# Optimization experiments

Hardware: AMD Instinct MI355X
Metric: run time of the kernel (lower is better)

## Reference

```python
import jax, jax.numpy as jnp
import numpy as np

N, F, H, R, T, E, C = 50000, 128, 64, 3, 2, 500000, 2


def _seg_sum(v, idx, n):
    return jax.ops.segment_sum(v, idx, num_segments=n)


def _sage(x, src, dst, Wl, Wr, b, n):
    # PyG SAGEConv(mean): lin_l(mean_{j->i} x_j) + lin_r(x_i); lin_l carries bias.
    s = _seg_sum(x[src], dst, n)
    cnt = _seg_sum(jnp.ones((src.shape[0],), x.dtype), dst, n)
    agg = s / jnp.maximum(cnt, 1.0)[:, None]
    return agg @ Wl + x @ Wr + b


def _gcn(x, src, dst, w, W, b, n):
    # PyG GCNConv with edge_weight: self-loops (weight 1) + symmetric norm.
    deg = _seg_sum(w, dst, n) + 1.0
    dinv = deg ** -0.5
    norm = dinv[src] * w * dinv[dst]
    xW = x @ W
    return _seg_sum(norm[:, None] * xW[src], dst, n) + xW / deg[:, None] + b


def setup_inputs() -> dict:
    key = jax.random.key(0)
    ks = jax.random.split(key, 32)
    rn = lambda k, shp, s=0.1: jax.random.normal(k, shp, dtype=jnp.float32) * s
    return {
        "x": rn(ks[0], (N, F), 1.0),
        "edge_main": jax.random.randint(ks[1], (R, 2, E), 0, N, dtype=jnp.int32),
        "edge_tree": jax.random.randint(ks[2], (R, T, 2, E), 0, N, dtype=jnp.int32),
        "sage_Wl0": rn(ks[3], (R, F, H)), "sage_Wr0": rn(ks[4], (R, F, H)), "sage_b0": rn(ks[5], (R, H)),
        "sage_Wl1": rn(ks[6], (R, H, H)), "sage_Wr1": rn(ks[7], (R, H, H)), "sage_b1": rn(ks[8], (R, H)),
        "tree_Wl": rn(ks[9], (R, T, F, H)), "tree_Wr": rn(ks[10], (R, T, F, H)), "tree_b": rn(ks[11], (R, T, H)),
        "gate_W": rn(ks[12], (R, T, H)), "gate_b": rn(ks[13], (R, T)),
        "node_emb": rn(ks[14], (R, H), 1.0), "edge_emb": rn(ks[15], (R, H), 1.0),
        "fm_W": rn(ks[16], (R, 2 * H + F, F)), "fm_b": rn(ks[17], (R, F)),
        "ea_W1": rn(ks[18], (3 * H, F)), "ea_b1": rn(ks[19], (F,)),
        "ea_W2": rn(ks[20], (F, 1)), "ea_b2": rn(ks[21], (1,)),
        "gcn_W0": rn(ks[22], (R, F, H)), "gcn_b0": rn(ks[23], (R, H)),
        "gcn_W1": rn(ks[24], (R, H, H)), "gcn_b1": rn(ks[25], (R, H)),
        "lin_W": rn(ks[26], (R * H, C)), "lin_b": rn(ks[27], (C,)),
    }


def reference(x, edge_main, edge_tree, sage_Wl0, sage_Wr0, sage_b0, sage_Wl1, sage_Wr1, sage_b1,
              tree_Wl, tree_Wr, tree_b, gate_W, gate_b, node_emb, edge_emb, fm_W, fm_b,
              ea_W1, ea_b1, ea_W2, ea_b2, gcn_W0, gcn_b0, gcn_W1, gcn_b1, lin_W, lin_b):
    outs = []
    for r in range(R):
        src, dst = edge_main[r, 0], edge_main[r, 1]
        # Layer_AGG main SAGE stack (2 layers, relu between; dropout = eval no-op)
        y = jax.nn.relu(_sage(x, src, dst, sage_Wl0[r], sage_Wr0[r], sage_b0[r], N))
        y = _sage(y, src, dst, sage_Wl1[r], sage_Wr1[r], sage_b1[r], N)
        # tree branches + softmax gating
        trees = []
        for t in range(T):
            ts, td = edge_tree[r, t, 0], edge_tree[r, t, 1]
            trees.append(jax.nn.relu(_sage(x, ts, td, tree_Wl[r, t], tree_Wr[r, t], tree_b[r, t], N)))
        gates = jnp.stack([trees[t] @ gate_W[r, t] + gate_b[r, t] for t in range(T)], axis=-1)  # [N,T]
        alpha = jax.nn.softmax(gates, axis=-1)
        x_tree = sum(trees[t] * alpha[:, t:t + 1] for t in range(T))
        lo = y + 1.0 * x_tree  # self.weight = 1
        # edge mask via edge_attr_mlp on [lo[src], lo[dst], edge_type_emb]
        ef = jnp.concatenate([lo[src], lo[dst], jnp.broadcast_to(edge_emb[r], (E, H))], axis=-1)
        em = jax.nn.relu(ef @ ea_W1 + ea_b1) @ ea_W2 + ea_b2  # [E,1]
        # feature mask via feat_mask_r on [lo, x, node_type_emb]
        hetro = jnp.concatenate([lo, x, jnp.broadcast_to(node_emb[r], (N, H))], axis=-1)
        fm = hetro @ fm_W[r] + fm_b[r]
        mx = x * fm
        w = ((em - em.min()) / (em.max() - em.min()))[:, 0]  # min-max norm -> [E]
        # hetero GCN stack with edge weights
        z = jax.nn.relu(_gcn(mx, src, dst, w, gcn_W0[r], gcn_b0[r], N))
        z = _gcn(z, src, dst, w, gcn_W1[r], gcn_b1[r], N)
        outs.append(z)
    x_temp = jnp.concatenate(outs, axis=1)  # [N, R*H]
    logits = jnp.clip(x_temp @ lin_W + lin_b, -1e10, 1e10)
    return jax.nn.log_softmax(logits, axis=1), x_temp
```

## Files before the change

### kernel.cpp

```cpp
#include <hip/hip_runtime.h>
#include <cstdint>

#define N_NODES 50000
#define FEAT    128
#define HID     64
#define NREL    3
#define NTREE   2
#define NEDGE   500000
#define NCLS    2

#define BKT   391
#define CAP   1600
#define CHUNK 4096

typedef __attribute__((ext_vector_type(8))) short bfrag;
typedef __attribute__((ext_vector_type(4))) float ffrag;

__device__ __forceinline__ float wave_red(float v){
  #pragma unroll
  for(int off = 32; off > 0; off >>= 1) v += __shfl_xor(v, off, 64);
  return v;
}

__device__ __forceinline__ unsigned short f2b(float f){
  unsigned int u = __float_as_uint(f);
  unsigned int r = (u + 0x7FFFu + ((u >> 16) & 1u)) >> 16;
  return (unsigned short)r;
}
__device__ __forceinline__ float b2f_lo(unsigned int u){ return __uint_as_float(u << 16); }
__device__ __forceinline__ float b2f_hi(unsigned int u){ return __uint_as_float(u & 0xFFFF0000u); }
__device__ __forceinline__ float b2f(unsigned short s){ return __uint_as_float(((unsigned int)s) << 16); }
__device__ __forceinline__ unsigned int pk2(float lo, float hi){
  return ((unsigned int)f2b(hi) << 16) | f2b(lo);
}

struct EdgePtrs { const int* s[9]; const int* d[9]; };

__global__ __launch_bounds__(256)
void k_passA(EdgePtrs ep, int* __restrict__ cursor, int* __restrict__ bucketed){
  int set = blockIdx.y;
  const int* src = ep.s[set];
  const int* dst = ep.d[set];
  __shared__ int stage[CHUNK];
  __shared__ int hist[BKT], gbase[BKT], lbase[BKT], cur[BKT];
  int tid = threadIdx.x;
  for(int b = tid; b < BKT; b += 256) hist[b] = 0;
  __syncthreads();
  int e0 = blockIdx.x * CHUNK;
  int nE = NEDGE - e0; if(nE > CHUNK) nE = CHUNK;
  for(int i = tid; i < nE; i += 256) atomicAdd(&hist[dst[e0 + i] >> 7], 1);
  __syncthreads();
  for(int b = tid; b < BKT; b += 256){
    int c = hist[b];
    gbase[b] = c ? atomicAdd(&cursor[set * BKT + b], c) : 0;
  }
  if(tid < 64){
    int running = 0;
    for(int base = 0; base < BKT; base += 64){
      int idx = base + tid;
      int v = (idx < BKT) ? hist[idx] : 0;
      int orig = v;
      #pragma unroll
      for(int off = 1; off < 64; off <<= 1){
        int t = __shfl_up(v, off, 64);
        if(tid >= off) v += t;
      }
      if(idx < BKT){ lbase[idx] = running + v - orig; cur[idx] = running + v - orig; }
      running += __shfl(v, 63, 64);
    }
  }
  __syncthreads();
  for(int i = tid; i < nE; i += 256){
    int e = e0 + i;
    int d = dst[e];
    int r = atomicAdd(&cur[d >> 7], 1);
    stage[r] = (d << 16) | src[e];
  }
  __syncthreads();
  int* bk = bucketed + (size_t)set * BKT * CAP;
  for(int i = tid; i < nE; i += 256){
    int p = stage[i];
    int b = ((unsigned int)p) >> 23;
    int pos = gbase[b] + (i - lbase[b]);
    if(pos < CAP) bk[b * CAP + pos] = p;
  }
}

__global__ void k_scanB(const int* __restrict__ cursor, int* __restrict__ bktbase,
                        int* __restrict__ indptr9){
  int set = blockIdx.x;
  __shared__ int sm[512];
  int tid = threadIdx.x;
  int v = (tid < BKT) ? cursor[set * BKT + tid] : 0;
  sm[tid] = v; __syncthreads();
  for(int off = 1; off < 512; off <<= 1){
    int t = (tid >= off) ? sm[tid - off] : 0;
    __syncthreads();
    sm[tid] += t;
    __syncthreads();
  }
  if(tid < BKT) bktbase[set * BKT + tid] = sm[tid] - v;
  if(tid == 0) indptr9[(size_t)set * (N_NODES + 1) + N_NODES] = NEDGE;
}

__global__ __launch_bounds__(256)
void k_passB(const int* __restrict__ bucketed, const int* __restrict__ cursor,
             const int* __restrict__ bktbase, int* __restrict__ indptr9,
             int* __restrict__ csr9){
  int set = blockIdx.y, b = blockIdx.x;
  int cnt = cursor[set * BKT + b]; if(cnt > CAP) cnt = CAP;
  int ebase = bktbase[set * BKT + b];
  const int* bk = bucketed + (size_t)set * BKT * CAP + b * CAP;
  __shared__ int pk[CAP];
  __shared__ int stage[CAP];
  __shared__ int h[128], sc[128], cur[128];
  int tid = threadIdx.x;
  for(int i = tid; i < cnt; i += 256) pk[i] = bk[i];
  if(tid < 128) h[tid] = 0;
  __syncthreads();
  for(int i = tid; i < cnt; i += 256) atomicAdd(&h[(pk[i] >> 16) & 127], 1);
  __syncthreads();
  if(tid < 128) sc[tid] = h[tid];
  __syncthreads();
  for(int off = 1; off < 128; off <<= 1){
    int t = 0;
    if(tid < 128 && tid >= off) t = sc[tid - off];
    __syncthreads();
    if(tid < 128) sc[tid] += t;
    __syncthreads();
  }
  if(tid < 128){
    int excl = sc[tid] - h[tid];
    cur[tid] = excl;
    int node = b * 128 + tid;
    if(node < N_NODES) indptr9[(size_t)set * (N_NODES + 1) + node] = ebase + excl;
  }
  __syncthreads();
  for(int i = tid; i < cnt; i += 256){
    int p = pk[i];
    int r = atomicAdd(&cur[(p >> 16) & 127], 1);
    stage[r] = p & 0xFFFF;
  }
  __syncthreads();
  int* out = csr9 + (size_t)set * NEDGE + ebase;
  for(int i = tid; i < cnt; i += 256) out[i] = stage[i];
}

__global__ void k_tobf16(const float* __restrict__ in, unsigned short* __restrict__ o, int n4){
  int i = blockIdx.x * 256 + threadIdx.x;
  if(i < n4){
    float4 v = ((const float4*)in)[i];
    ushort4 u; u.x = f2b(v.x); u.y = f2b(v.y); u.z = f2b(v.z); u.w = f2b(v.w);
    ((ushort4*)o)[i] = u;
  }
}

struct PackJobs { const float* src[20]; int wst[20]; int K[20]; int dst[20]; int n; };

__global__ void k_wpack(PackJobs J, unsigned short* __restrict__ out){
  int j = blockIdx.x;
  if(j >= J.n) return;
  const float* s = J.src[j];
  int wst = J.wst[j], K = J.K[j];
  unsigned short* o = out + J.dst[j];
  for(int i = threadIdx.x; i < K * 64; i += 256){
    int k = i >> 6, c = i & 63;
    o[((((k >> 3) * 64) + c) << 3) + (k & 7)] = f2b(s[(size_t)k * wst + c]);
  }
}

struct MG {
  const unsigned short* Wt[4];
  const float* bias[4];
  const void* add[4];
  const float* mul[4];
  void* out[4];
  int ast, mst, ost;
};

template<int K1, int NGRP, int OUT_BF16>
__global__ __launch_bounds__(256)
void k_mgemm(const unsigned short* __restrict__ X1, int xs1, MG P){
  constexpr int KS = K1 / 32;
  int tid = threadIdx.x;
  int lane = tid & 63;
  int w = tid >> 6;
  int row0 = blockIdx.x * 64 + w * 16;
  int l15 = lane & 15, kg = lane >> 4;
  int arow = row0 + l15; if(arow > N_NODES - 1) arow = N_NODES - 1;
  bfrag a[KS];
  #pragma unroll
  for(int ks = 0; ks < KS; ks++)
    a[ks] = *(const bfrag*)(X1 + (size_t)arow * xs1 + ks * 32 + kg * 8);
  int orow0 = row0 + kg * 4;
  #pragma unroll
  for(int g = 0; g < NGRP; g++){
    const unsigned short* Wg = P.Wt[g];
    #pragma unroll
    for(int ct = 0; ct < 4; ct++){
      int col = ct * 16 + l15;
      ffrag acc = {0.f, 0.f, 0.f, 0.f};
      #pragma unroll
      for(int ks = 0; ks < KS; ks++){
        bfrag bf = *(const bfrag*)(Wg + (((size_t)(ks * 4 + kg) * 64 + col) << 3));
        acc = __builtin_amdgcn_mfma_f32_16x16x32_bf16(a[ks], bf, acc, 0, 0, 0);
      }
      #pragma unroll
      for(int i = 0; i < 4; i++){
        int r = orow0 + i;
        if(r >= N_NODES) break;
        float v = acc[i];
        if(OUT_BF16) ((unsigned short*)P.out[g])[(size_t)r * P.ost + col] = f2b(v);
        else         ((float*)P.out[g])[(size_t)r * P.ost + col] = v;
      }
    }
  }
}

struct S23 {
  const unsigned short* Wr[3];
  const float* bias[3];
  const unsigned short* ag3;
  const unsigned short* Wl1;
  unsigned short *y0, *t0, *t1, *tbs;
};

__global__ __launch_bounds__(256)
void k_s23(const unsigned short* __restrict__ xb, S23 P){
  __shared__ unsigned short ytile[64][72];
  int tid = threadIdx.x, lane = tid & 63, w = tid >> 6;
  int row0 = blockIdx.x * 64 + w * 16;
  int l15 = lane & 15, kg = lane >> 4;
  int arow = row0 + l15; if(arow > N_NODES - 1) arow = N_NODES - 1;
  bfrag a[4];
  #pragma unroll
  for(int ks = 0; ks < 4; ks++)
    a[ks] = *(const bfrag*)(xb + (size_t)arow * 128 + ks * 32 + kg * 8);
  int orow0 = row0 + kg * 4;
  #pragma unroll
  for(int g = 0; g < 3; g++){
    const unsigned short* Wg = P.Wr[g];
    unsigned short* og = (g == 0) ? P.y0 : (g == 1) ? P.t0 : P.t1;
    #pragma unroll
    for(int ct = 0; ct < 4; ct++){
      int col = ct * 16 + l15;
      ffrag acc = {0.f, 0.f, 0.f, 0.f};
      #pragma unroll
      for(int ks = 0; ks < 4; ks++){
        bfrag bf = *(const bfrag*)(Wg + (((size_t)(ks * 4 + kg) * 64 + col) << 3));
        acc = __builtin_amdgcn_mfma_f32_16x16x32_bf16(a[ks], bf, acc, 0, 0, 0);
      }
      float bv = P.bias[g][col];
      #pragma unroll
      for(int i = 0; i < 4; i++){
        int r = orow0 + i;
        int rr = (r < N_NODES) ? r : N_NODES - 1;
        float v = acc[i] + bv + b2f(P.ag3[(size_t)g * N_NODES * 64 + (size_t)rr * 64 + col]);
        v = fmaxf(v, 0.f);
        unsigned short hh = f2b(v);
        if(g == 0) ytile[w * 16 + kg * 4 + i][col] = hh;
        if(r < N_NODES) og[(size_t)r * 64 + col] = hh;
      }
    }
  }
  __syncthreads();
  bfrag a2[2];
  a2[0] = *(const bfrag*)&ytile[w * 16 + l15][kg * 8];
  a2[1] = *(const bfrag*)&ytile[w * 16 + l15][32 + kg * 8];
  #pragma unroll
  for(int ct = 0; ct < 4; ct++){
    int col = ct * 16 + l15;
    ffrag acc = {0.f, 0.f, 0.f, 0.f};
    bfrag b0 = *(const bfrag*)(P.Wl1 + (((size_t)(0 * 4 + kg) * 64 + col) << 3));
    bfrag b1 = *(const bfrag*)(P.Wl1 + (((size_t)(1 * 4 + kg) * 64 + col) << 3));
    acc = __builtin_amdgcn_mfma_f32_16x16x32_bf16(a2[0], b0, acc, 0, 0, 0);
    acc = __builtin_amdgcn_mfma_f32_16x16x32_bf16(a2[1], b1, acc, 0, 0, 0);
    #pragma unroll
    for(int i = 0; i < 4; i++){
      int r = orow0 + i;
      if(r >= N_NODES) break;
      P.tbs[(size_t)r * 64 + col] = f2b(acc[i]);
    }
  }
}

struct YG {
  const unsigned short* Wr1;
  const float* b1;
  const float* AG;
  const unsigned short *t0b, *t1b;
  const float *gate_W, *gate_b;
  unsigned short* lo;
  const float *ee, *ne, *eaW1, *eab1, *fmW, *fmb;
  float *cE, *cF;
  int ggm;
};

__global__ __launch_bounds__(256)
void k_ygates(const unsigned short* __restrict__ y0b, YG P){
  if(blockIdx.x >= P.ggm){
    int which = blockIdx.x - P.ggm;
    int j = threadIdx.x;
    if(j < 128){
      if(which == 0){
        float s = P.eab1[j];
        for(int k = 0; k < 64; k++) s += P.ee[k] * P.eaW1[(128 + k) * 128 + j];
        P.cE[j] = s;
      } else {
        float s = P.fmb[j];
        for(int k = 0; k < 64; k++) s += P.ne[k] * P.fmW[(192 + k) * 128 + j];
        P.cF[j] = s;
      }
    }
    return;
  }
  int tid = threadIdx.x, lane = tid & 63, w = tid >> 6;
  int row0 = blockIdx.x * 64 + w * 16;
  int l15 = lane & 15, kg = lane >> 4;
  int arow = row0 + l15; if(arow > N_NODES - 1) arow = N_NODES - 1;
  bfrag a0f = *(const bfrag*)(y0b + (size_t)arow * 64 + kg * 8);
  bfrag a1f = *(const bfrag*)(y0b + (size_t)arow * 64 + 32 + kg * 8);
  int orow0 = row0 + kg * 4;
  float vv[4][4], t0v[4][4], t1v[4][4];
  float gw0[4], gw1[4];
  #pragma unroll
  for(int ct = 0; ct < 4; ct++){
    int col = ct * 16 + l15;
    gw0[ct] = P.gate_W[col];
    gw1[ct] = P.gate_W[64 + col];
  }
  #pragma unroll
  for(int ct = 0; ct < 4; ct++){
    int col = ct * 16 + l15;
    ffrag acc = {0.f, 0.f, 0.f, 0.f};
    bfrag b0 = *(const bfrag*)(P.Wr1 + (((size_t)(0 * 4 + kg) * 64 + col) << 3));
    bfrag b1 = *(const bfrag*)(P.Wr1 + (((size_t)(1 * 4 + kg) * 64 + col) << 3));
    acc = __builtin_amdgcn_mfma_f32_16x16x32_bf16(a0f, b0, acc, 0, 0, 0);
    acc = __builtin_amdgcn_mfma_f32_16x16x32_bf16(a1f, b1, acc, 0, 0, 0);
    float bv = P.b1[col];
    #pragma unroll
    for(int i = 0; i < 4; i++){
      int r = orow0 + i;
      int rr = (r < N_NODES) ? r : N_NODES - 1;
      vv[i][ct] = acc[i] + bv + P.AG[(size_t)rr * 64 + col];
      t0v[i][ct] = b2f(P.t0b[(size_t)rr * 64 + col]);
      t1v[i][ct] = b2f(P.t1b[(size_t)rr * 64 + col]);
    }
  }
  float pg0[4] = {0.f, 0.f, 0.f, 0.f}, pg1[4] = {0.f, 0.f, 0.f, 0.f};
  #pragma unroll
  for(int i = 0; i < 4; i++)
    #pragma unroll
    for(int ct = 0; ct < 4; ct++){
      pg0[i] += t0v[i][ct] * gw0[ct];
      pg1[i] += t1v[i][ct] * gw1[ct];
    }
  #pragma unroll
  for(int off = 1; off < 16; off <<= 1){
    #pragma unroll
    for(int i = 0; i < 4; i++){
      pg0[i] += __shfl_xor(pg0[i], off, 64);
      pg1[i] += __shfl_xor(pg1[i], off, 64);
    }
  }
  float gb0 = P.gate_b[0], gb1 = P.gate_b[1];
  #pragma unroll
  for(int i = 0; i < 4; i++){
    int r = orow0 + i;
    if(r >= N_NODES) break;
    float g0 = pg0[i] + gb0, g1 = pg1[i] + gb1;
    float m = fmaxf(g0, g1);
    float e0 = expf(g0 - m), e1 = expf(g1 - m);
    float av = e0 / (e0 + e1);
    #pragma unroll
    for(int ct = 0; ct < 4; ct++){
      int col = ct * 16 + l15;
      P.lo[(size_t)r * 64 + col] = f2b(vv[i][ct] + av * t0v[i][ct] + (1.f - av) * t1v[i][ct]);
    }
  }
}

struct ABMX2 {
  const unsigned short* Wea[4];
  const unsigned short* Wfm[2];
  const unsigned short* G0;
  const float* cF;
  const float* xf32;
  unsigned short* ab;
  unsigned short* xw0;
};

__global__ __launch_bounds__(256)
void k_abmx2(const unsigned short* __restrict__ LOb, const unsigned short* __restrict__ xb, ABMX2 P){
  __shared__ unsigned short mxtile[64][136];
  int tid = threadIdx.x, lane = tid & 63, w = tid >> 6;
  int row0 = blockIdx.x * 64 + w * 16;
  int l15 = lane & 15, kg = lane >> 4;
  int arow = row0 + l15; if(arow > N_NODES - 1) arow = N_NODES - 1;
  bfrag a[6];
  a[0] = *(const bfrag*)(LOb + (size_t)arow * 64 + kg * 8);
  a[1] = *(const bfrag*)(LOb + (size_t)arow * 64 + 32 + kg * 8);
  #pragma unroll
  for(int ks = 0; ks < 4; ks++)
    a[2 + ks] = *(const bfrag*)(xb + (size_t)arow * 128 + ks * 32 + kg * 8);
  int orow0 = row0 + kg * 4;
  #pragma unroll
  for(int g = 0; g < 4; g++){
    const unsigned short* Wg = P.Wea[g];
    #pragma unroll
    for(int ct = 0; ct < 4; ct++){
      int col = ct * 16 + l15;
      ffrag acc = {0.f, 0.f, 0.f, 0.f};
      bfrag b0 = *(const bfrag*)(Wg + (((size_t)(0 * 4 + kg) * 64 + col) << 3));
      bfrag b1 = *(const bfrag*)(Wg + (((size_t)(1 * 4 + kg) * 64 + col) << 3));
      acc = __builtin_amdgcn_mfma_f32_16x16x32_bf16(a[0], b0, acc, 0, 0, 0);
      acc = __builtin_amdgcn_mfma_f32_16x16x32_bf16(a[1], b1, acc, 0, 0, 0);
      #pragma unroll
      for(int i = 0; i < 4; i++){
        int r = orow0 + i;
        if(r >= N_NODES) break;
        P.ab[(size_t)r * 256 + g * 64 + col] = f2b(acc[i]);
      }
    }
  }
  #pragma unroll
  for(int g = 0; g < 2; g++){
    const unsigned short* Wg = P.Wfm[g];
    #pragma unroll
    for(int ct = 0; ct < 4; ct++){
      int col = ct * 16 + l15;
      ffrag acc = {0.f, 0.f, 0.f, 0.f};
      #pragma unroll
      for(int ks = 0; ks < 6; ks++){
        bfrag bf = *(const bfrag*)(Wg + (((size_t)(ks * 4 + kg) * 64 + col) << 3));
        acc = __builtin_amdgcn_mfma_f32_16x16x32_bf16(a[ks], bf, acc, 0, 0, 0);
      }
      float bv = P.cF[g * 64 + col];
      #pragma unroll
      for(int i = 0; i < 4; i++){
        int r = orow0 + i;
        int rr = (r < N_NODES) ? r : N_NODES - 1;
        float v = (acc[i] + bv) * P.xf32[(size_t)rr * 128 + g * 64 + col];
        mxtile[w * 16 + kg * 4 + i][g * 64 + col] = f2b(v);
      }
    }
  }
  __syncthreads();
  bfrag a3[4];
  #pragma unroll
  for(int ks = 0; ks < 4; ks++)
    a3[ks] = *(const bfrag*)&mxtile[w * 16 + l15][ks * 32 + kg * 8];
  #pragma unroll
  for(int ct = 0; ct < 4; ct++){
    int col = ct * 16 + l15;
    ffrag acc = {0.f, 0.f, 0.f, 0.f};
    #pragma unroll
    for(int ks = 0; ks < 4; ks++){
      bfrag bf = *(const bfrag*)(P.G0 + (((size_t)(ks * 4 + kg) * 64 + col) << 3));
      acc = __builtin_amdgcn_mfma_f32_16x16x32_bf16(a3[ks], bf, acc, 0, 0, 0);
    }
    #pragma unroll
    for(int i = 0; i < 4; i++){
      int r = orow0 + i;
      if(r >= N_NODES) break;
      P.xw0[(size_t)r * 64 + col] = f2b(acc[i]);
    }
  }
}

template<int OUTB>
__global__ void k_aggq(const unsigned short* __restrict__ TB, int tst,
                       const int* __restrict__ indptr, const int* __restrict__ csr,
                       void* __restrict__ out){
  int br = blockIdx.y;
  const unsigned short* T = TB + (size_t)br * tst;
  const int* ip = indptr + (size_t)br * (N_NODES + 1);
  const int* cs = csr + (size_t)br * NEDGE;
  int lane = threadIdx.x & 63, wid = threadIdx.x >> 6;
  int node = blockIdx.x * 4 + wid;
  if(node >= N_NODES) return;
  int q = lane >> 4, c = lane & 15;
  int beg = ip[node], end = ip[node + 1];
  int cnt = end - beg;
  float sc = 1.0f / (float)(cnt >= 1 ? cnt : 1);
  float a0 = 0.f, a1 = 0.f, a2 = 0.f, a3 = 0.f;
  int j = beg + q;
  for(; j + 4 < end; j += 8){
    int s0 = cs[j], s1 = cs[j + 4];
    uint2 u0 = *(const uint2*)(T + (size_t)s0 * 64 + c * 4);
    uint2 u1 = *(const uint2*)(T + (size_t)s1 * 64 + c * 4);
    a0 += b2f_lo(u0.x) + b2f_lo(u1.x); a1 += b2f_hi(u0.x) + b2f_hi(u1.x);
    a2 += b2f_lo(u0.y) + b2f_lo(u1.y); a3 += b2f_hi(u0.y) + b2f_hi(u1.y);
  }
  if(j < end){
    int s = cs[j];
    uint2 u = *(const uint2*)(T + (size_t)s * 64 + c * 4);
    a0 += b2f_lo(u.x); a1 += b2f_hi(u.x);
    a2 += b2f_lo(u.y); a3 += b2f_hi(u.y);
  }
  a0 += __shfl_xor(a0, 16, 64); a1 += __shfl_xor(a1, 16, 64);
  a2 += __shfl_xor(a2, 16, 64); a3 += __shfl_xor(a3, 16, 64);
  a0 += __shfl_xor(a0, 32, 64); a1 += __shfl_xor(a1, 32, 64);
  a2 += __shfl_xor(a2, 32, 64); a3 += __shfl_xor(a3, 32, 64);
  if(q == 0){
    if(OUTB){
      ushort4 o; o.x = f2b(a0 * sc); o.y = f2b(a1 * sc); o.z = f2b(a2 * sc); o.w = f2b(a3 * sc);
      *(ushort4*)((unsigned short*)out + (size_t)br * tst + (size_t)node * 64 + c * 4) = o;
    } else {
      *(float4*)((float*)out + (size_t)node * 64 + c * 4) = float4{a0 * sc, a1 * sc, a2 * sc, a3 * sc};
    }
  }
}

__global__ void k_em2(const unsigned short* __restrict__ AB,
                      const int* __restrict__ indptr, const int* __restrict__ csr_src,
                      const float* __restrict__ cvec, const float* __restrict__ W2,
                      const float* __restrict__ b2, float* __restrict__ em,
                      float* __restrict__ sumem, float* __restrict__ pmn, float* __restrict__ pmx){
  int lane = threadIdx.x & 63, wid = threadIdx.x >> 6;
  int node = blockIdx.x * 4 + wid;
  float mn = 3.4e38f, mx = -3.4e38f;
  if(node < N_NODES){
    int q = lane >> 4, c = lane & 15;
    uint4 bu = *(const uint4*)(AB + (size_t)node * 256 + 128 + c * 8);
    float4 cva = *(const float4*)&cvec[c * 8];
    float4 cvb = *(const float4*)&cvec[c * 8 + 4];
    float4 wva = *(const float4*)&W2[c * 8];
    float4 wvb = *(const float4*)&W2[c * 8 + 4];
    float cc0 = b2f_lo(bu.x) + cva.x, cc1 = b2f_hi(bu.x) + cva.y;
    float cc2 = b2f_lo(bu.y) + cva.z, cc3 = b2f_hi(bu.y) + cva.w;
    float cc4 = b2f_lo(bu.z) + cvb.x, cc5 = b2f_hi(bu.z) + cvb.y;
    float cc6 = b2f_lo(bu.w) + cvb.z, cc7 = b2f_hi(bu.w) + cvb.w;
    float b2v = b2[0];
    int beg = indptr[node], end = indptr[node + 1];
    float ssum = 0.f;
    int j = beg + q;
    for(; j + 4 < end; j += 8){
      int s0 = csr_src[j], s1 = csr_src[j + 4];
      uint4 u0 = *(const uint4*)(AB + (size_t)s0 * 256 + c * 8);
      uint4 u1 = *(const uint4*)(AB + (size_t)s1 * 256 + c * 8);
      float v0 = fmaxf(b2f_lo(u0.x) + cc0, 0.f) * wva.x + fmaxf(b2f_hi(u0.x) + cc1, 0.f) * wva.y
               + fmaxf(b2f_lo(u0.y) + cc2, 0.f) * wva.z + fmaxf(b2f_hi(u0.y) + cc3, 0.f) * wva.w
               + fmaxf(b2f_lo(u0.z) + cc4, 0.f) * wvb.x + fmaxf(b2f_hi(u0.z) + cc5, 0.f) * wvb.y
               + fmaxf(b2f_lo(u0.w) + cc6, 0.f) * wvb.z + fmaxf(b2f_hi(u0.w) + cc7, 0.f) * wvb.w;
      float v1 = fmaxf(b2f_lo(u1.x) + cc0, 0.f) * wva.x + fmaxf(b2f_hi(u1.x) + cc1, 0.f) * wva.y
               + fmaxf(b2f_lo(u1.y) + cc2, 0.f) * wva.z + fmaxf(b2f_hi(u1.y) + cc3, 0.f) * wva.w
               + fmaxf(b2f_lo(u1.z) + cc4, 0.f) * wvb.x + fmaxf(b2f_hi(u1.z) + cc5, 0.f) * wvb.y
               + fmaxf(b2f_lo(u1.w) + cc6, 0.f) * wvb.z + fmaxf(b2f_hi(u1.w) + cc7, 0.f) * wvb.w;
      #pragma unroll
      for(int off = 1; off < 16; off <<= 1){
        v0 += __shfl_xor(v0, off, 64);
        v1 += __shfl_xor(v1, off, 64);
      }
      float r0 = v0 + b2v, r1 = v1 + b2v;
      if(c == 0){ em[j] = r0; em[j + 4] = r1; }
      ssum += r0 + r1;
      mn = fminf(mn, fminf(r0, r1)); mx = fmaxf(mx, fmaxf(r0, r1));
    }
    if(j < end){
      int s = csr_src[j];
      uint4 u = *(const uint4*)(AB + (size_t)s * 256 + c * 8);
      float v = fmaxf(b2f_lo(u.x) + cc0, 0.f) * wva.x + fmaxf(b2f_hi(u.x) + cc1, 0.f) * wva.y
              + fmaxf(b2f_lo(u.y) + cc2, 0.f) * wva.z + fmaxf(b2f_hi(u.y) + cc3, 0.f) * wva.w
              + fmaxf(b2f_lo(u.z) + cc4, 0.f) * wvb.x + fmaxf(b2f_hi(u.z) + cc5, 0.f) * wvb.y
              + fmaxf(b2f_lo(u.w) + cc6, 0.f) * wvb.z + fmaxf(b2f_hi(u.w) + cc7, 0.f) * wvb.w;
      #pragma unroll
      for(int off = 1; off < 16; off <<= 1) v += __shfl_xor(v, off, 64);
      float r = v + b2v;
      if(c == 0) em[j] = r;
      ssum += r;
      mn = fminf(mn, r); mx = fmaxf(mx, r);
    }
    ssum += __shfl_xor(ssum, 16, 64); ssum += __shfl_xor(ssum, 32, 64);
    mn = fminf(mn, __shfl_xor(mn, 16, 64)); mn = fminf(mn, __shfl_xor(mn, 32, 64));
    mx = fmaxf(mx, __shfl_xor(mx, 16, 64)); mx = fmaxf(mx, __shfl_xor(mx, 32, 64));
    if(lane == 0) sumem[node] = ssum;
  }
  __shared__ float bmn[4], bmx[4];
  if(lane == 0){ bmn[wid] = mn; bmx[wid] = mx; }
  __syncthreads();
  if(threadIdx.x == 0){
    pmn[blockIdx.x] = fminf(fminf(bmn[0], bmn[1]), fminf(bmn[2], bmn[3]));
    pmx[blockIdx.x] = fmaxf(fmaxf(bmx[0], bmx[1]), fmaxf(bmx[2], bmx[3]));
  }
}

__global__ void k_dinv2(const int* __restrict__ indptr, const float* __restrict__ sumem,
                        const float* __restrict__ pmn, const float* __restrict__ pmx, int nb,
                        float* __restrict__ scal, float* __restrict__ dinv){
  __shared__ float smn[256], smx[256];
  int tid = threadIdx.x;
  float mn = 3.4e38f, mx = -3.4e38f;
  for(int i = tid; i < nb; i += 256){
    mn = fminf(mn, pmn[i]); mx = fmaxf(mx, pmx[i]);
  }
  smn[tid] = mn; smx[tid] = mx; __syncthreads();
  for(int s = 128; s > 0; s >>= 1){
    if(tid < s){ smn[tid] = fminf(smn[tid], smn[tid + s]); smx[tid] = fmaxf(smx[tid], smx[tid + s]); }
    __syncthreads();
  }
  float mn0 = smn[0];
  float inv = 1.0f / fmaxf(smx[0] - mn0, 1e-30f);
  if(blockIdx.x == 0 && tid == 0){ scal[0] = mn0; scal[1] = inv; }
  int i = blockIdx.x * 256 + tid;
  if(i >= N_NODES) return;
  float cnt = (float)(indptr[i + 1] - indptr[i]);
  dinv[i] = rsqrtf(1.f + (sumem[i] - cnt * mn0) * inv);
}

template<int RELU, int OUTB>
__global__ void k_gcn(const unsigned short* __restrict__ xW, const int* __restrict__ indptr,
                      const int* __restrict__ csr_src, const float* __restrict__ em,
                      const float* __restrict__ scal, const float* __restrict__ dinv,
                      const float* __restrict__ bias, void* __restrict__ out, int ostride){
  int lane = threadIdx.x & 63, wid = threadIdx.x >> 6;
  int node = blockIdx.x * 4 + wid;
  if(node >= N_NODES) return;
  int q = lane >> 3, c = lane & 7;
  float mn = scal[0], inv = scal[1];
  float di = dinv[node];
  float a0=0.f,a1=0.f,a2=0.f,a3=0.f,a4=0.f,a5=0.f,a6=0.f,a7=0.f;
  int beg = indptr[node], end = indptr[node + 1];
  int j = beg + q;
  for(; j + 8 < end; j += 16){
    int s0 = csr_src[j], s1 = csr_src[j + 8];
    float w0 = (em[j] - mn) * inv * dinv[s0];
    float w1 = (em[j + 8] - mn) * inv * dinv[s1];
    uint4 u0 = *(const uint4*)(xW + (size_t)s0 * 64 + c * 8);
    uint4 u1 = *(const uint4*)(xW + (size_t)s1 * 64 + c * 8);
    a0 += w0 * b2f_lo(u0.x) + w1 * b2f_lo(u1.x); a1 += w0 * b2f_hi(u0.x) + w1 * b2f_hi(u1.x);
    a2 += w0 * b2f_lo(u0.y) + w1 * b2f_lo(u1.y); a3 += w0 * b2f_hi(u0.y) + w1 * b2f_hi(u1.y);
    a4 += w0 * b2f_lo(u0.z) + w1 * b2f_lo(u1.z); a5 += w0 * b2f_hi(u0.z) + w1 * b2f_hi(u1.z);
    a6 += w0 * b2f_lo(u0.w) + w1 * b2f_lo(u1.w); a7 += w0 * b2f_hi(u0.w) + w1 * b2f_hi(u1.w);
  }
  if(j < end){
    int s = csr_src[j];
    float wv = (em[j] - mn) * inv * dinv[s];
    uint4 u = *(const uint4*)(xW + (size_t)s * 64 + c * 8);
    a0 += wv * b2f_lo(u.x); a1 += wv * b2f_hi(u.x);
    a2 += wv * b2f_lo(u.y); a3 += wv * b2f_hi(u.y);
    a4 += wv * b2f_lo(u.z); a5 += wv * b2f_hi(u.z);
    a6 += wv * b2f_lo(u.w); a7 += wv * b2f_hi(u.w);
  }
  #pragma unroll
  for(int off = 8; off < 64; off <<= 1){
    a0 += __shfl_xor(a0, off, 64); a1 += __shfl_xor(a1, off, 64);
    a2 += __shfl_xor(a2, off, 64); a3 += __shfl_xor(a3, off, 64);
    a4 += __shfl_xor(a4, off, 64); a5 += __shfl_xor(a5, off, 64);
    a6 += __shfl_xor(a6, off, 64); a7 += __shfl_xor(a7, off, 64);
  }
  if(q == 0){
    uint4 su = *(const uint4*)(xW + (size_t)node * 64 + c * 8);
    float4 bva = *(const float4*)&bias[c * 8];
    float4 bvb = *(const float4*)&bias[c * 8 + 4];
    float dd = di * di;
    float r0 = a0 * di + b2f_lo(su.x) * dd + bva.x;
    float r1 = a1 * di + b2f_hi(su.x) * dd + bva.y;
    float r2 = a2 * di + b2f_lo(su.y) * dd + bva.z;
    float r3 = a3 * di + b2f_hi(su.y) * dd + bva.w;
    float r4 = a4 * di + b2f_lo(su.z) * dd + bvb.x;
    float r5 = a5 * di + b2f_hi(su.z) * dd + bvb.y;
    float r6 = a6 * di + b2f_lo(su.w) * dd + bvb.z;
    float r7 = a7 * di + b2f_hi(su.w) * dd + bvb.w;
    if(RELU){
      r0 = fmaxf(r0, 0.f); r1 = fmaxf(r1, 0.f); r2 = fmaxf(r2, 0.f); r3 = fmaxf(r3, 0.f);
      r4 = fmaxf(r4, 0.f); r5 = fmaxf(r5, 0.f); r6 = fmaxf(r6, 0.f); r7 = fmaxf(r7, 0.f);
    }
    if(OUTB){
      uint4 o;
      o.x = pk2(r0, r1); o.y = pk2(r2, r3); o.z = pk2(r4, r5); o.w = pk2(r6, r7);
      *(uint4*)((unsigned short*)out + (size_t)node * ostride + c * 8) = o;
    } else {
      float* o = (float*)out + (size_t)node * ostride + c * 8;
      *(float4*)o       = float4{r0, r1, r2, r3};
      *(float4*)(o + 4) = float4{r4, r5, r6, r7};
    }
  }
}

__global__ void k_logits(const float* __restrict__ xt, const float* __restrict__ lin_W,
                         const float* __restrict__ lin_b, float* __restrict__ out){
  int lane = threadIdx.x & 63, wid = threadIdx.x >> 6;
  int node = blockIdx.x * 4 + wid;
  if(node >= N_NODES) return;
  float a0 = 0.f, a1 = 0.f;
  #pragma unroll
  for(int q = 0; q < 3; q++){
    int k = q * 64 + lane;
    float v = xt[(size_t)node * 192 + k];
    a0 += v * lin_W[k * 2 + 0];
    a1 += v * lin_W[k * 2 + 1];
  }
  a0 = wave_red(a0);
  a1 = wave_red(a1);
  if(lane == 0){
    float l0 = fminf(fmaxf(a0 + lin_b[0], -1e10f), 1e10f);
    float l1 = fminf(fmaxf(a1 + lin_b[1], -1e10f), 1e10f);
    float m = fmaxf(l0, l1);
    float d = expf(l0 - m) + expf(l1 - m);
    float ls = m + logf(d);
    out[(size_t)node * 2 + 0] = l0 - ls;
    out[(size_t)node * 2 + 1] = l1 - ls;
  }
}

extern "C" void kernel_launch(void* const* d_in, const int* in_sizes, int n_in,
                              void* d_out, int out_size, void* d_ws, size_t ws_size,
                              hipStream_t stream){
  (void)in_sizes; (void)n_in; (void)out_size;
  const int N = N_NODES, E = NEDGE;

  const float* x        = (const float*)d_in[0];
  const int*  edge_main = (const int*)d_in[1];
  const int*  edge_tree = (const int*)d_in[2];
  const float* sage_Wl0 = (const float*)d_in[3];
  const float* sage_Wr0 = (const float*)d_in[4];
  const float* sage_b0  = (const float*)d_in[5];
  const float* sage_Wl1 = (const float*)d_in[6];
  const float* sage_Wr1 = (const float*)d_in[7];
  const float* sage_b1  = (const float*)d_in[8];
  const float* tree_Wl  = (const float*)d_in[9];
  const float* tree_Wr  = (const float*)d_in[10];
  const float* tree_b   = (const float*)d_in[11];
  const float* gate_W   = (const float*)d_in[12];
  const float* gate_b   = (const float*)d_in[13];
  const float* node_emb = (const float*)d_in[14];
  const float* edge_emb = (const float*)d_in[15];
  const float* fm_W     = (const float*)d_in[16];
  const float* fm_b     = (const float*)d_in[17];
  const float* ea_W1    = (const float*)d_in[18];
  const float* ea_b1    = (const float*)d_in[19];
  const float* ea_W2    = (const float*)d_in[20];
  const float* ea_b2    = (const float*)d_in[21];
  const float* gcn_W0   = (const float*)d_in[22];
  const float* gcn_b0   = (const float*)d_in[23];
  const float* gcn_W1   = (const float*)d_in[24];
  const float* gcn_b1   = (const float*)d_in[25];
  const float* lin_W    = (const float*)d_in[26];
  const float* lin_b    = (const float*)d_in[27];

  float* out_lsm   = (float*)d_out;
  float* out_xtemp = (float*)d_out + (size_t)N * NCLS;

  char* ws = (char*)d_ws;
  unsigned short* TB3  = (unsigned short*)(ws + 0);
  unsigned short* TBs  = (unsigned short*)(ws + 0);
  unsigned short* AB   = (unsigned short*)(ws + 0);
  unsigned short* AG3  = (unsigned short*)(ws + 19200000);
  float*          AG   = (float*)(ws + 19200000);
  unsigned short* LOb  = (unsigned short*)(ws + 32000000);
  unsigned short* y0b  = (unsigned short*)(ws + 38400000);
  unsigned short* xW0b = (unsigned short*)(ws + 38400000);
  unsigned short* T0b  = (unsigned short*)(ws + 44800000);
  unsigned short* z0b  = (unsigned short*)(ws + 44800000);
  unsigned short* T1b  = (unsigned short*)(ws + 51200000);
  unsigned short* xW1b = (unsigned short*)(ws + 51200000);
  unsigned short* xb   = (unsigned short*)(ws + 57600000);
  int*   bucketed = (int*)(ws + 0);
  unsigned short* Wpk = (unsigned short*)(ws + 70400000);
  int*   csr9     = (int*)(ws + 71000064);
  int*   indptr9  = (int*)(ws + 89000064);
  float* em       = (float*)(ws + 90800128);
  float* sumem    = (float*)(ws + 92800128);
  float* dinv     = (float*)(ws + 93000128);
  int*   cursor   = (int*)(ws + 93200128);
  int*   bktbase  = (int*)(ws + 93214208);
  float* cvecE    = (float*)(ws + 93228288);
  float* cvecF    = (float*)(ws + 93228800);
  float* scal     = (float*)(ws + 93229312);
  float* pmn      = (float*)(ws + 93229568);
  float* pmx      = (float*)(ws + 93279568);
  if(ws_size < 93330000) return;

  const int GN4 = (N + 3) / 4;
  const int GN  = (N + 255) / 256;
  const int GGM = (N + 63) / 64;
  const int NCH = (E + CHUNK - 1) / CHUNK;

  PackJobs PJ[2]; PJ[0].n = 0; PJ[1].n = 0;
  int npj = 0, dstElem = 0;
  const unsigned short* WlpA[NREL]; const unsigned short* WlpB[NREL]; const unsigned short* WlpC[NREL];
  const unsigned short* Wr0j[NREL]; const unsigned short* WrT0[NREL]; const unsigned short* WrT1[NREL];
  const unsigned short* Wl1j[NREL]; const unsigned short* Wr1j[NREL];
  const unsigned short* Fm0j[NREL]; const unsigned short* Fm1j[NREL];
  const unsigned short* G0j[NREL];  const unsigned short* G1j[NREL];
  const unsigned short *EaA0, *EaA1, *EaB0, *EaB1;
  auto addjob = [&](const float* src, int wst, int K) -> const unsigned short* {
    int slot = npj < 20 ? 0 : 1;
    int k = npj - slot * 20;
    PJ[slot].src[k] = src; PJ[slot].wst[k] = wst; PJ[slot].K[k] = K; PJ[slot].dst[k] = dstElem;
    PJ[slot].n = k + 1;
    const unsigned short* ret = Wpk + dstElem;
    dstElem += K * 64; npj++;
    return ret;
  };
  for(int r = 0; r < NREL; r++){
    WlpA[r] = addjob(sage_Wl0 + (size_t)r * 8192, 64, 128);
    WlpB[r] = addjob(tree_Wl + (size_t)(r * NTREE + 0) * 8192, 64, 128);
    WlpC[r] = addjob(tree_Wl + (size_t)(r * NTREE + 1) * 8192, 64, 128);
    Wr0j[r] = addjob(sage_Wr0 + (size_t)r * 8192, 64, 128);
    WrT0[r] = addjob(tree_Wr + (size_t)(r * NTREE + 0) * 8192, 64, 128);
    WrT1[r] = addjob(tree_Wr + (size_t)(r * NTREE + 1) * 8192, 64, 128);
    Wl1j[r] = addjob(sage_Wl1 + (size_t)r * 4096, 64, 64);
    Wr1j[r] = addjob(sage_Wr1 + (size_t)r * 4096, 64, 64);
    Fm0j[r] = addjob(fm_W + (size_t)r * 32768, 128, 192);
    Fm1j[r] = addjob(fm_W + (size_t)r * 32768 + 64, 128, 192);
    G0j[r]  = addjob(gcn_W0 + (size_t)r * 8192, 64, 128);
    G1j[r]  = addjob(gcn_W1 + (size_t)r * 4096, 64, 64);
  }
  EaA0 = addjob(ea_W1, 128, 64);
  EaA1 = addjob(ea_W1 + 64, 128, 64);
  EaB0 = addjob(ea_W1 + 64 * 128, 128, 64);
  EaB1 = addjob(ea_W1 + 64 * 128 + 64, 128, 64);

  EdgePtrs ep;
  for(int r = 0; r < NREL; r++){
    ep.s[r * 3 + 0] = edge_main + (size_t)r * 2 * E;
    ep.d[r * 3 + 0] = ep.s[r * 3 + 0] + E;
    for(int t = 0; t < NTREE; t++){
      ep.s[r * 3 + 1 + t] = edge_tree + ((size_t)(r * NTREE + t) * 2) * E;
      ep.d[r * 3 + 1 + t] = ep.s[r * 3 + 1 + t] + E;
    }
  }
  hipMemsetAsync(cursor, 0, 9 * BKT * 4, stream);
  k_passA<<<dim3(NCH, 9), 256, 0, stream>>>(ep, cursor, bucketed);
  k_scanB<<<9, 512, 0, stream>>>(cursor, bktbase, indptr9);
  k_passB<<<dim3(BKT, 9), 256, 0, stream>>>(bucketed, cursor, bktbase, indptr9, csr9);

  k_wpack<<<PJ[0].n, 256, 0, stream>>>(PJ[0], Wpk);
  k_wpack<<<PJ[1].n, 256, 0, stream>>>(PJ[1], Wpk);
  k_tobf16<<<(N * 128 / 4 + 255) / 256, 256, 0, stream>>>(x, xb, N * 128 / 4);

  for(int r = 0; r < NREL; r++){
    const int* ipM = indptr9 + (size_t)(r * 3) * (N + 1);
    const int* csM = csr9 + (size_t)(r * 3) * E;

    { MG p{}; p.ost = 64;
      p.Wt[0] = WlpA[r]; p.Wt[1] = WlpB[r]; p.Wt[2] = WlpC[r];
      p.out[0] = TB3; p.out[1] = TB3 + (size_t)N * 64; p.out[2] = TB3 + (size_t)2 * N * 64;
      k_mgemm<128, 3, 1><<<GGM, 256, 0, stream>>>(xb, 128, p); }

    k_aggq<1><<<dim3(GN4, 3), 256, 0, stream>>>(TB3, N * 64, ipM, csM, AG3);

    { S23 p{};
      p.Wr[0] = Wr0j[r]; p.bias[0] = sage_b0 + r * 64;
      p.Wr[1] = WrT0[r]; p.bias[1] = tree_b + (size_t)(r * NTREE + 0) * 64;
      p.Wr[2] = WrT1[r]; p.bias[2] = tree_b + (size_t)(r * NTREE + 1) * 64;
      p.ag3 = AG3; p.Wl1 = Wl1j[r];
      p.y0 = y0b; p.t0 = T0b; p.t1 = T1b; p.tbs = TBs;
      k_s23<<<GGM, 256, 0, stream>>>(xb, p); }

    k_aggq<0><<<dim3(GN4, 1), 256, 0, stream>>>(TBs, N * 64, ipM, csM, AG);

    { YG p{};
      p.Wr1 = Wr1j[r]; p.b1 = sage_b1 + r * 64; p.AG = AG;
      p.t0b = T0b; p.t1b = T1b;
      p.gate_W = gate_W + (size_t)r * 128; p.gate_b = gate_b + r * 2;
      p.lo = LOb;
      p.ee = edge_emb + r * 64; p.ne = node_emb + r * 64;
      p.eaW1 = ea_W1; p.eab1 = ea_b1;
      p.fmW = fm_W + (size_t)r * 32768; p.fmb = fm_b + r * 128;
      p.cE = cvecE; p.cF = cvecF; p.ggm = GGM;
      k_ygates<<<GGM + 2, 256, 0, stream>>>(y0b, p); }

    { ABMX2 p{};
      p.Wea[0] = EaA0; p.Wea[1] = EaA1; p.Wea[2] = EaB0; p.Wea[3] = EaB1;
      p.Wfm[0] = Fm0j[r]; p.Wfm[1] = Fm1j[r];
      p.G0 = G0j[r]; p.cF = cvecF; p.xf32 = x;
      p.ab = AB; p.xw0 = xW0b;
      k_abmx2<<<GGM, 256, 0, stream>>>(LOb, xb, p); }

    k_em2<<<GN4, 256, 0, stream>>>(AB, ipM, csM, cvecE, ea_W2, ea_b2, em, sumem, pmn, pmx);

    k_dinv2<<<GN, 256, 0, stream>>>(ipM, sumem, pmn, pmx, GN4, scal, dinv);

    k_gcn<1, 1><<<GN4, 256, 0, stream>>>(xW0b, ipM, csM, em, scal, dinv, gcn_b0 + r * 64, z0b, 64);
    { MG p{}; p.ost = 64; p.Wt[0] = G1j[r]; p.out[0] = xW1b;
      k_mgemm<64, 1, 1><<<GGM, 256, 0, stream>>>(z0b, 64, p); }
    k_gcn<0, 0><<<GN4, 256, 0, stream>>>(xW1b, ipM, csM, em, scal, dinv, gcn_b1 + r * 64,
                                         out_xtemp + r * 64, 192);
  }

  k_logits<<<GN4, 256, 0, stream>>>(out_xtemp, lin_W, lin_b, out_lsm);
}
```

Before: 799.5 us.

## Precompute per-edge GCN weights and pack float math into 2-wide vectors

Adds a k_wedge kernel that computes each edge's normalized GCN weight (min-max scaled edge mask times dinv[src]) once per relation. Both GCN layers then read this single array instead of recomputing the weight from em, scal and a random dinv gather. Separately, the aggregation, edge-MLP and GCN inner loops are rewritten with float2 vectors so the compiler can emit packed FP32 ops, and shuffles move pairs as 64-bit values. This costs an extra launch and a 2 MB weight array, and relies on the compiler actually producing packed math.

```diff
diff --git a/kernel.cpp b/kernel.cpp
--- a/kernel.cpp
+++ b/kernel.cpp
@@ -15,6 +15,7 @@
 
 typedef __attribute__((ext_vector_type(8))) short bfrag;
 typedef __attribute__((ext_vector_type(4))) float ffrag;
+typedef __attribute__((ext_vector_type(2))) float f32x2;
 
 __device__ __forceinline__ float wave_red(float v){
   #pragma unroll
@@ -32,6 +33,21 @@
 __device__ __forceinline__ float b2f(unsigned short s){ return __uint_as_float(((unsigned int)s) << 16); }
 __device__ __forceinline__ unsigned int pk2(float lo, float hi){
   return ((unsigned int)f2b(hi) << 16) | f2b(lo);
+}
+__device__ __forceinline__ f32x2 up2(unsigned int u){
+  f32x2 r; r.x = __uint_as_float(u << 16); r.y = __uint_as_float(u & 0xFFFF0000u); return r;
+}
+__device__ __forceinline__ f32x2 mk2(float a, float b){ f32x2 r; r.x = a; r.y = b; return r; }
+__device__ __forceinline__ f32x2 shfl_xor2(f32x2 v, int off){
+  double d = __shfl_xor(*(double*)&v, off, 64);
+  return *(f32x2*)&d;
+}
+__device__ __forceinline__ f32x2 vmax2(f32x2 a, f32x2 b){
+#if __has_builtin(__builtin_elementwise_max)
+  return __builtin_elementwise_max(a, b);
+#else
+  f32x2 r; r.x = fmaxf(a.x, b.x); r.y = fmaxf(a.y, b.y); return r;
+#endif
 }
 
 struct EdgePtrs { const int* s[9]; const int* d[9]; };
@@ -483,31 +499,31 @@
   int beg = ip[node], end = ip[node + 1];
   int cnt = end - beg;
   float sc = 1.0f / (float)(cnt >= 1 ? cnt : 1);
-  float a0 = 0.f, a1 = 0.f, a2 = 0.f, a3 = 0.f;
+  f32x2 a01 = mk2(0.f, 0.f), a23 = mk2(0.f, 0.f);
   int j = beg + q;
   for(; j + 4 < end; j += 8){
     int s0 = cs[j], s1 = cs[j + 4];
     uint2 u0 = *(const uint2*)(T + (size_t)s0 * 64 + c * 4);
     uint2 u1 = *(const uint2*)(T + (size_t)s1 * 64 + c * 4);
-    a0 += b2f_lo(u0.x) + b2f_lo(u1.x); a1 += b2f_hi(u0.x) + b2f_hi(u1.x);
-    a2 += b2f_lo(u0.y) + b2f_lo(u1.y); a3 += b2f_hi(u0.y) + b2f_hi(u1.y);
+    a01 += up2(u0.x); a01 += up2(u1.x);
+    a23 += up2(u0.y); a23 += up2(u1.y);
   }
   if(j < end){
     int s = cs[j];
     uint2 u = *(const uint2*)(T + (size_t)s * 64 + c * 4);
-    a0 += b2f_lo(u.x); a1 += b2f_hi(u.x);
-    a2 += b2f_lo(u.y); a3 += b2f_hi(u.y);
-  }
-  a0 += __shfl_xor(a0, 16, 64); a1 += __shfl_xor(a1, 16, 64);
-  a2 += __shfl_xor(a2, 16, 64); a3 += __shfl_xor(a3, 16, 64);
-  a0 += __shfl_xor(a0, 32, 64); a1 += __shfl_xor(a1, 32, 64);
-  a2 += __shfl_xor(a2, 32, 64); a3 += __shfl_xor(a3, 32, 64);
+    a01 += up2(u.x);
+    a23 += up2(u.y);
+  }
+  a01 += shfl_xor2(a01, 16); a23 += shfl_xor2(a23, 16);
+  a01 += shfl_xor2(a01, 32); a23 += shfl_xor2(a23, 32);
   if(q == 0){
     if(OUTB){
-      ushort4 o; o.x = f2b(a0 * sc); o.y = f2b(a1 * sc); o.z = f2b(a2 * sc); o.w = f2b(a3 * sc);
+      ushort4 o; o.x = f2b(a01.x * sc); o.y = f2b(a01.y * sc);
+      o.z = f2b(a23.x * sc); o.w = f2b(a23.y * sc);
       *(ushort4*)((unsigned short*)out + (size_t)br * tst + (size_t)node * 64 + c * 4) = o;
     } else {
-      *(float4*)((float*)out + (size_t)node * 64 + c * 4) = float4{a0 * sc, a1 * sc, a2 * sc, a3 * sc};
+      *(float4*)((float*)out + (size_t)node * 64 + c * 4) =
+        float4{a01.x * sc, a01.y * sc, a23.x * sc, a23.y * sc};
     }
   }
 }
@@ -527,10 +543,13 @@
     float4 cvb = *(const float4*)&cvec[c * 8 + 4];
     float4 wva = *(const float4*)&W2[c * 8];
     float4 wvb = *(const float4*)&W2[c * 8 + 4];
-    float cc0 = b2f_lo(bu.x) + cva.x, cc1 = b2f_hi(bu.x) + cva.y;
-    float cc2 = b2f_lo(bu.y) + cva.z, cc3 = b2f_hi(bu.y) + cva.w;
-    float cc4 = b2f_lo(bu.z) + cvb.x, cc5 = b2f_hi(bu.z) + cvb.y;
-    float cc6 = b2f_lo(bu.w) + cvb.z, cc7 = b2f_hi(bu.w) + cvb.w;
+    const f32x2 z2 = mk2(0.f, 0.f);
+    f32x2 ccx = up2(bu.x) + mk2(cva.x, cva.y);
+    f32x2 ccy = up2(bu.y) + mk2(cva.z, cva.w);
+    f32x2 ccz = up2(bu.z) + mk2(cvb.x, cvb.y);
+    f32x2 ccw = up2(bu.w) + mk2(cvb.z, cvb.w);
+    f32x2 wx = mk2(wva.x, wva.y), wy = mk2(wva.z, wva.w);
+    f32x2 wz = mk2(wvb.x, wvb.y), ww = mk2(wvb.z, wvb.w);
     float b2v = b2[0];
     int beg = indptr[node], end = indptr[node + 1];
     float ssum = 0.f;
@@ -539,20 +558,20 @@
       int s0 = csr_src[j], s1 = csr_src[j + 4];
       uint4 u0 = *(const uint4*)(AB + (size_t)s0 * 256 + c * 8);
       uint4 u1 = *(const uint4*)(AB + (size_t)s1 * 256 + c * 8);
-      float v0 = fmaxf(b2f_lo(u0.x) + cc0, 0.f) * wva.x + fmaxf(b2f_hi(u0.x) + cc1, 0.f) * wva.y
-               + fmaxf(b2f_lo(u0.y) + cc2, 0.f) * wva.z + fmaxf(b2f_hi(u0.y) + cc3, 0.f) * wva.w
-               + fmaxf(b2f_lo(u0.z) + cc4, 0.f) * wvb.x + fmaxf(b2f_hi(u0.z) + cc5, 0.f) * wvb.y
-               + fmaxf(b2f_lo(u0.w) + cc6, 0.f) * wvb.z + fmaxf(b2f_hi(u0.w) + cc7, 0.f) * wvb.w;
-      float v1 = fmaxf(b2f_lo(u1.x) + cc0, 0.f) * wva.x + fmaxf(b2f_hi(u1.x) + cc1, 0.f) * wva.y
-               + fmaxf(b2f_lo(u1.y) + cc2, 0.f) * wva.z + fmaxf(b2f_hi(u1.y) + cc3, 0.f) * wva.w
-               + fmaxf(b2f_lo(u1.z) + cc4, 0.f) * wvb.x + fmaxf(b2f_hi(u1.z) + cc5, 0.f) * wvb.y
-               + fmaxf(b2f_lo(u1.w) + cc6, 0.f) * wvb.z + fmaxf(b2f_hi(u1.w) + cc7, 0.f) * wvb.w;
+      f32x2 p0 = vmax2(up2(u0.x) + ccx, z2) * wx;
+      p0 += vmax2(up2(u0.y) + ccy, z2) * wy;
+      p0 += vmax2(up2(u0.z) + ccz, z2) * wz;
+      p0 += vmax2(up2(u0.w) + ccw, z2) * ww;
+      f32x2 p1 = vmax2(up2(u1.x) + ccx, z2) * wx;
+      p1 += vmax2(up2(u1.y) + ccy, z2) * wy;
+      p1 += vmax2(up2(u1.z) + ccz, z2) * wz;
+      p1 += vmax2(up2(u1.w) + ccw, z2) * ww;
       #pragma unroll
       for(int off = 1; off < 16; off <<= 1){
-        v0 += __shfl_xor(v0, off, 64);
-        v1 += __shfl_xor(v1, off, 64);
+        p0 += shfl_xor2(p0, off);
+        p1 += shfl_xor2(p1, off);
       }
-      float r0 = v0 + b2v, r1 = v1 + b2v;
+      float r0 = p0.x + p0.y + b2v, r1 = p1.x + p1.y + b2v;
       if(c == 0){ em[j] = r0; em[j + 4] = r1; }
       ssum += r0 + r1;
       mn = fminf(mn, fminf(r0, r1)); mx = fmaxf(mx, fmaxf(r0, r1));
@@ -560,13 +579,13 @@
     if(j < end){
       int s = csr_src[j];
       uint4 u = *(const uint4*)(AB + (size_t)s * 256 + c * 8);
-      float v = fmaxf(b2f_lo(u.x) + cc0, 0.f) * wva.x + fmaxf(b2f_hi(u.x) + cc1, 0.f) * wva.y
-              + fmaxf(b2f_lo(u.y) + cc2, 0.f) * wva.z + fmaxf(b2f_hi(u.y) + cc3, 0.f) * wva.w
-              + fmaxf(b2f_lo(u.z) + cc4, 0.f) * wvb.x + fmaxf(b2f_hi(u.z) + cc5, 0.f) * wvb.y
-              + fmaxf(b2f_lo(u.w) + cc6, 0.f) * wvb.z + fmaxf(b2f_hi(u.w) + cc7, 0.f) * wvb.w;
+      f32x2 p = vmax2(up2(u.x) + ccx, z2) * wx;
+      p += vmax2(up2(u.y) + ccy, z2) * wy;
+      p += vmax2(up2(u.z) + ccz, z2) * wz;
+      p += vmax2(up2(u.w) + ccw, z2) * ww;
       #pragma unroll
-      for(int off = 1; off < 16; off <<= 1) v += __shfl_xor(v, off, 64);
-      float r = v + b2v;
+      for(int off = 1; off < 16; off <<= 1) p += shfl_xor2(p, off);
+      float r = p.x + p.y + b2v;
       if(c == 0) em[j] = r;
       ssum += r;
       mn = fminf(mn, r); mx = fmaxf(mx, r);
@@ -608,60 +627,67 @@
   dinv[i] = rsqrtf(1.f + (sumem[i] - cnt * mn0) * inv);
 }
 
+__global__ void k_wedge(const int* __restrict__ csr_src, const float* __restrict__ em,
+                        const float* __restrict__ dinv, const float* __restrict__ scal,
+                        float* __restrict__ we){
+  int j = blockIdx.x * 256 + threadIdx.x;
+  if(j >= NEDGE) return;
+  we[j] = (em[j] - scal[0]) * scal[1] * dinv[csr_src[j]];
+}
+
 template<int RELU, int OUTB>
 __global__ void k_gcn(const unsigned short* __restrict__ xW, const int* __restrict__ indptr,
-                      const int* __restrict__ csr_src, const float* __restrict__ em,
-                      const float* __restrict__ scal, const float* __restrict__ dinv,
-                      const float* __restrict__ bias, void* __restrict__ out, int ostride){
+                      const int* __restrict__ csr_src, const float* __restrict__ we,
+                      const float* __restrict__ dinv, const float* __restrict__ bias,
+                      void* __restrict__ out, int ostride){
   int lane = threadIdx.x & 63, wid = threadIdx.x >> 6;
   int node = blockIdx.x * 4 + wid;
   if(node >= N_NODES) return;
   int q = lane >> 3, c = lane & 7;
-  float mn = scal[0], inv = scal[1];
   float di = dinv[node];
-  float a0=0.f,a1=0.f,a2=0.f,a3=0.f,a4=0.f,a5=0.f,a6=0.f,a7=0.f;
+  f32x2 a01 = mk2(0.f, 0.f), a23 = mk2(0.f, 0.f), a45 = mk2(0.f, 0.f), a67 = mk2(0.f, 0.f);
   int beg = indptr[node], end = indptr[node + 1];
   int j = beg + q;
   for(; j + 8 < end; j += 16){
     int s0 = csr_src[j], s1 = csr_src[j + 8];
-    float w0 = (em[j] - mn) * inv * dinv[s0];
-    float w1 = (em[j + 8] - mn) * inv * dinv[s1];
+    float t0 = we[j], t1 = we[j + 8];
+    f32x2 w0 = mk2(t0, t0), w1 = mk2(t1, t1);
     uint4 u0 = *(const uint4*)(xW + (size_t)s0 * 64 + c * 8);
     uint4 u1 = *(const uint4*)(xW + (size_t)s1 * 64 + c * 8);
-    a0 += w0 * b2f_lo(u0.x) + w1 * b2f_lo(u1.x); a1 += w0 * b2f_hi(u0.x) + w1 * b2f_hi(u1.x);
-    a2 += w0 * b2f_lo(u0.y) + w1 * b2f_lo(u1.y); a3 += w0 * b2f_hi(u0.y) + w1 * b2f_hi(u1.y);
-    a4 += w0 * b2f_lo(u0.z) + w1 * b2f_lo(u1.z); a5 += w0 * b2f_hi(u0.z) + w1 * b2f_hi(u1.z);
-    a6 += w0 * b2f_lo(u0.w) + w1 * b2f_lo(u1.w); a7 += w0 * b2f_hi(u0.w) + w1 * b2f_hi(u1.w);
+    a01 += w0 * up2(u0.x); a01 += w1 * up2(u1.x);
+    a23 += w0 * up2(u0.y); a23 += w1 * up2(u1.y);
+    a45 += w0 * up2(u0.z); a45 += w1 * up2(u1.z);
+    a67 += w0 * up2(u0.w); a67 += w1 * up2(u1.w);
   }
   if(j < end){
     int s = csr_src[j];
-    float wv = (em[j] - mn) * inv * dinv[s];
+    float t = we[j];
+    f32x2 w = mk2(t, t);
     uint4 u = *(const uint4*)(xW + (size_t)s * 64 + c * 8);
-    a0 += wv * b2f_lo(u.x); a1 += wv * b2f_hi(u.x);
-    a2 += wv * b2f_lo(u.y); a3 += wv * b2f_hi(u.y);
-    a4 += wv * b2f_lo(u.z); a5 += wv * b2f_hi(u.z);
-    a6 += wv * b2f_lo(u.w); a7 += wv * b2f_hi(u.w);
+    a01 += w * up2(u.x);
+    a23 += w * up2(u.y);
+    a45 += w * up2(u.z);
+    a67 += w * up2(u.w);
   }
   #pragma unroll
   for(int off = 8; off < 64; off <<= 1){
-    a0 += __shfl_xor(a0, off, 64); a1 += __shfl_xor(a1, off, 64);
-    a2 += __shfl_xor(a2, off, 64); a3 += __shfl_xor(a3, off, 64);
-    a4 += __shfl_xor(a4, off, 64); a5 += __shfl_xor(a5, off, 64);
-    a6 += __shfl_xor(a6, off, 64); a7 += __shfl_xor(a7, off, 64);
+    a01 += shfl_xor2(a01, off); a23 += shfl_xor2(a23, off);
+    a45 += shfl_xor2(a45, off); a67 += shfl_xor2(a67, off);
   }
   if(q == 0){
     uint4 su = *(const uint4*)(xW + (size_t)node * 64 + c * 8);
     float4 bva = *(const float4*)&bias[c * 8];
     float4 bvb = *(const float4*)&bias[c * 8 + 4];
     float dd = di * di;
-    float r0 = a0 * di + b2f_lo(su.x) * dd + bva.x;
-    float r1 = a1 * di + b2f_hi(su.x) * dd + bva.y;
-    float r2 = a2 * di + b2f_lo(su.y) * dd + bva.z;
-    float r3 = a3 * di + b2f_hi(su.y) * dd + bva.w;
-    float r4 = a4 * di + b2f_lo(su.z) * dd + bvb.x;
-    float r5 = a5 * di + b2f_hi(su.z) * dd + bvb.y;
-    float r6 = a6 * di + b2f_lo(su.w) * dd + bvb.z;
-    float r7 = a7 * di + b2f_hi(su.w) * dd + bvb.w;
+    f32x2 sx = up2(su.x), sy = up2(su.y), sz = up2(su.z), sw = up2(su.w);
+    float r0 = a01.x * di + sx.x * dd + bva.x;
+    float r1 = a01.y * di + sx.y * dd + bva.y;
+    float r2 = a23.x * di + sy.x * dd + bva.z;
+    float r3 = a23.y * di + sy.y * dd + bva.w;
+    float r4 = a45.x * di + sz.x * dd + bvb.x;
+    float r5 = a45.y * di + sz.y * dd + bvb.y;
+    float r6 = a67.x * di + sw.x * dd + bvb.z;
+    float r7 = a67.y * di + sw.y * dd + bvb.w;
     if(RELU){
       r0 = fmaxf(r0, 0.f); r1 = fmaxf(r1, 0.f); r2 = fmaxf(r2, 0.f); r3 = fmaxf(r3, 0.f);
       r4 = fmaxf(r4, 0.f); r5 = fmaxf(r5, 0.f); r6 = fmaxf(r6, 0.f); r7 = fmaxf(r7, 0.f);
@@ -770,11 +796,13 @@
   float* scal     = (float*)(ws + 93229312);
   float* pmn      = (float*)(ws + 93229568);
   float* pmx      = (float*)(ws + 93279568);
-  if(ws_size < 93330000) return;
+  float* we       = (float*)(ws + 93330176);
+  if(ws_size < 95340000) return;
 
   const int GN4 = (N + 3) / 4;
   const int GN  = (N + 255) / 256;
   const int GGM = (N + 63) / 64;
+  const int GE2 = (E + 255) / 256;
   const int NCH = (E + CHUNK - 1) / CHUNK;
 
   PackJobs PJ[2]; PJ[0].n = 0; PJ[1].n = 0;
@@ -874,10 +902,12 @@
 
     k_dinv2<<<GN, 256, 0, stream>>>(ipM, sumem, pmn, pmx, GN4, scal, dinv);
 
-    k_gcn<1, 1><<<GN4, 256, 0, stream>>>(xW0b, ipM, csM, em, scal, dinv, gcn_b0 + r * 64, z0b, 64);
+    k_wedge<<<GE2, 256, 0, stream>>>(csM, em, dinv, scal, we);
+
+    k_gcn<1, 1><<<GN4, 256, 0, stream>>>(xW0b, ipM, csM, we, dinv, gcn_b0 + r * 64, z0b, 64);
     { MG p{}; p.ost = 64; p.Wt[0] = G1j[r]; p.out[0] = xW1b;
       k_mgemm<64, 1, 1><<<GGM, 256, 0, stream>>>(z0b, 64, p); }
-    k_gcn<0, 0><<<GN4, 256, 0, stream>>>(xW1b, ipM, csM, em, scal, dinv, gcn_b1 + r * 64,
+    k_gcn<0, 0><<<GN4, 256, 0, stream>>>(xW1b, ipM, csM, we, dinv, gcn_b1 + r * 64,
                                          out_xtemp + r * 64, 192);
   }
 
```

New measurement: 814.1 us. About the same (+1.8%).
